# Kernel optimization log

Measured on AMD Instinct MI355X. Metric: run time of the kernel, lower is better.

Reference implementation:

```python
import jax, jax.numpy as jnp
import numpy as np

D_MODEL = 384
N_HEADS = 8
HEAD_DIM = D_MODEL // N_HEADS


def setup_inputs() -> dict:
    key = jax.random.key(0)
    ks = jax.random.split(key, 8)
    b, n = 2, 2048
    s = 0.02
    return {
        "x": jax.random.normal(ks[0], (b, n, D_MODEL), jnp.float32),
        "coords": jax.random.normal(ks[1], (b, n, 3), jnp.float32),
        "W_qkv": jax.random.normal(ks[2], (D_MODEL, 3 * D_MODEL), jnp.float32) * s,
        "b_qkv": jnp.zeros((3 * D_MODEL,), jnp.float32),
        "W_dist": jax.random.normal(ks[3], (1, N_HEADS), jnp.float32) * s,
        "b_dist": jnp.zeros((N_HEADS,), jnp.float32),
        "W_out": jax.random.normal(ks[4], (D_MODEL, D_MODEL), jnp.float32) * s,
        "b_out": jnp.zeros((D_MODEL,), jnp.float32),
    }


def reference(x, coords, W_qkv, b_qkv, W_dist, b_dist, W_out, b_out):
    b, n, _ = x.shape
    qkv = x @ W_qkv + b_qkv                       # (b, n, 3*d)
    q, k, v = jnp.split(qkv, 3, axis=-1)
    def heads(t):
        return t.reshape(b, n, N_HEADS, HEAD_DIM).transpose(0, 2, 1, 3)  # b h n d
    q, k, v = heads(q), heads(k), heads(v)
    attn = jnp.einsum('bhid,bhjd->bhij', q, k) / jnp.sqrt(jnp.float32(HEAD_DIM))
    # distance bias: ||c_i - c_j|| projected to heads (Linear(1, n_heads))
    diff = coords[:, :, None, :] - coords[:, None, :, :]   # (b, i, j, 3)
    dist = jnp.sqrt(jnp.sum(diff * diff, axis=-1))         # (b, i, j)
    dist_bias = dist[..., None] * W_dist[0] + b_dist       # (b, i, j, h)
    attn = attn + dist_bias.transpose(0, 3, 1, 2)          # (b, h, i, j)
    attn = jax.nn.softmax(attn, axis=-1)
    out = jnp.einsum('bhij,bhjd->bhid', attn, v)
    out = out.transpose(0, 2, 1, 3).reshape(b, n, D_MODEL)
    return out @ W_out + b_out
```

## Files before the change

### kernel.cpp

```cpp
#include <hip/hip_runtime.h>
#include <hip/hip_bf16.h>

#define NB 2
#define SEQ 2048
#define DM 384
#define NH 8
#define HD 48
#define QKVN 1152
#define BH (NB*NH)
#define NSPLIT 4

typedef __hip_bfloat16 bf16;
typedef __attribute__((ext_vector_type(8))) short short8;
typedef __attribute__((ext_vector_type(4))) float float4v;

static __device__ __forceinline__ float bf2f(bf16 v){ return __bfloat162float(v); }
static __device__ __forceinline__ float ldin(const void* p, size_t i, int isf){
    return isf ? ((const float*)p)[i] : bf2f(((const bf16*)p)[i]);
}
static __device__ __forceinline__ short f2b(float f){
    union { float f; unsigned u; } a; a.f = f;
    unsigned r = a.u + 0x7FFFu + ((a.u >> 16) & 1u);
    return (short)(r >> 16);
}
static __device__ __forceinline__ unsigned pk2(float a, float b){
    union { float f; unsigned u; } ua, ub; ua.f = a; ub.f = b;
    return ((ua.u + 0x8000u) >> 16) | ((ub.u + 0x8000u) & 0xFFFF0000u);
}
static __device__ __forceinline__ float bflo(unsigned u){
    union { unsigned u; float f; } a; a.u = u << 16; return a.f;
}
static __device__ __forceinline__ float bfhi(unsigned u){
    union { unsigned u; float f; } a; a.u = u & 0xFFFF0000u; return a.f;
}
static __device__ __forceinline__ float bfs(unsigned short s){
    union { unsigned u; float f; } a; a.u = ((unsigned)s) << 16; return a.f;
}
static __device__ __forceinline__ int detect_isf(const void* x){
    const unsigned short* xb = (const unsigned short*)x;
    int l = threadIdx.x & 63;
    union { unsigned u; float f; } a; a.u = ((unsigned)xb[2*l]) << 16;
    float ab = fabsf(a.f);
    int good = (a.f == 0.0f) || (ab > 9.765625e-4f && ab < 1024.0f);
    unsigned long long m = __ballot(good);
    return (__popcll(m) >= 32) ? 0 : 1;
}

__global__ __launch_bounds__(256) void k_prep(const void* __restrict__ x,
    const void* __restrict__ coords,
    const void* __restrict__ Wqkv, const void* __restrict__ Wout,
    const void* __restrict__ bqkv, const void* __restrict__ bout,
    const void* __restrict__ Wdist, const void* __restrict__ bdist,
    short* __restrict__ dist8, short* __restrict__ xb,
    short* __restrict__ WqT, short* __restrict__ WoT,
    float* __restrict__ bqf, float* __restrict__ bof,
    float* __restrict__ wdf, float* __restrict__ bdf)
{
    const int isf = detect_isf(x);
    const int t = threadIdx.x;
    const int b = blockIdx.x;
    if (b < 512) {
        const int bb = b >> 8;
        const int j0 = (b & 255) * 8;
        __shared__ float cjx[8], cjy[8], cjz[8];
        if (t < 8) {
            int gj = (bb*SEQ + j0 + t)*3;
            cjx[t] = ldin(coords, gj, isf);
            cjy[t] = ldin(coords, gj+1, isf);
            cjz[t] = ldin(coords, gj+2, isf);
        }
        __syncthreads();
        #pragma unroll
        for (int ii = 0; ii < 8; ++ii) {
            int i = ii*256 + t;
            int gi = (bb*SEQ + i)*3;
            float px = ldin(coords, gi, isf), py = ldin(coords, gi+1, isf), pz = ldin(coords, gi+2, isf);
            short o[8];
            #pragma unroll
            for (int e = 0; e < 8; ++e) {
                float dx = px - cjx[e], dy = py - cjy[e], dz = pz - cjz[e];
                o[e] = f2b(sqrtf(dx*dx + dy*dy + dz*dz));
            }
            *(int4*)(dist8 + ((size_t)b*SEQ + i)*8) = *(const int4*)o;
        }
    } else if (b < 1280) {
        size_t i = ((size_t)(b-512)*256 + t)*8;
        if (isf) {
            const float* xf = (const float*)x + i;
            short o[8];
            #pragma unroll
            for (int e = 0; e < 8; ++e) o[e] = f2b(xf[e]);
            *(int4*)(xb + i) = *(const int4*)o;
        } else {
            *(int4*)(xb + i) = *(const int4*)((const short*)x + i);
        }
    } else if (b < 1856) {
        int bb, NW; const void* W; short* WT;
        if (b < 1712) { bb = b - 1280; NW = QKVN; W = Wqkv; WT = WqT; }
        else          { bb = b - 1712; NW = DM;   W = Wout; WT = WoT; }
        int ntiles = NW >> 5;
        int kt = bb / ntiles, nt = bb % ntiles;
        int k0 = kt*32, n0 = nt*32;
        __shared__ float Ls[32][33];
        for (int idx = t; idx < 1024; idx += 256) {
            int r = idx >> 5, c = idx & 31;
            Ls[r][c] = ldin(W, (size_t)(k0+r)*NW + n0 + c, isf);
        }
        __syncthreads();
        for (int idx = t; idx < 1024; idx += 256) {
            int r2 = idx >> 5, c2 = idx & 31;
            WT[(size_t)(n0+r2)*DM + k0 + c2] = f2b(Ls[c2][r2]);
        }
    } else {
        int idx = (b - 1856)*256 + t;
        if (idx < QKVN) bqf[idx] = ldin(bqkv, idx, isf);
        else if (idx < QKVN + DM) bof[idx - QKVN] = ldin(bout, idx - QKVN, isf);
        else if (idx < QKVN + DM + NH) wdf[idx - QKVN - DM] = ldin(Wdist, idx - QKVN - DM, isf);
        else if (idx < QKVN + DM + 2*NH) bdf[idx - QKVN - DM - NH] = ldin(bdist, idx - QKVN - DM - NH, isf);
    }
}

__global__ __launch_bounds__(256) void k_qkv(const short* __restrict__ xb,
    const short* __restrict__ WT, const float* __restrict__ bias,
    short* __restrict__ qg2, short* __restrict__ kg2, short* __restrict__ vg2)
{
    __shared__ __align__(16) short As[64*72];
    __shared__ __align__(16) short Bs[128*72];
    const int t = threadIdx.x;
    const int w = t >> 6, lane = t & 63, L = lane & 15, quad = lane >> 4;
    const int mt = blockIdx.x / 9, nt = blockIdx.x % 9;
    const int row0 = mt*64, col0 = nt*128;
    const int wm = w & 1, wn = w >> 1;
    float4v acc[2][4] = {};
    for (int k0 = 0; k0 < DM; k0 += 64) {
        __syncthreads();
        for (int c = t; c < 512; c += 256) {
            int row = c >> 3, k8 = c & 7;
            *(int4*)(&As[row*72 + k8*8]) = *(const int4*)(xb + (size_t)(row0+row)*DM + k0 + k8*8);
        }
        for (int c = t; c < 1024; c += 256) {
            int row = c >> 3, k8 = c & 7;
            *(int4*)(&Bs[row*72 + k8*8]) = *(const int4*)(WT + (size_t)(col0+row)*DM + k0 + k8*8);
        }
        __syncthreads();
        #pragma unroll
        for (int kc = 0; kc < 2; ++kc) {
            short8 a0 = *(const short8*)(&As[(32*wm + L)*72 + kc*32 + quad*8]);
            short8 a1 = *(const short8*)(&As[(32*wm + 16 + L)*72 + kc*32 + quad*8]);
            #pragma unroll
            for (int ni = 0; ni < 4; ++ni) {
                short8 bf = *(const short8*)(&Bs[(64*wn + 16*ni + L)*72 + kc*32 + quad*8]);
                acc[0][ni] = __builtin_amdgcn_mfma_f32_16x16x32_bf16(a0, bf, acc[0][ni], 0, 0, 0);
                acc[1][ni] = __builtin_amdgcn_mfma_f32_16x16x32_bf16(a1, bf, acc[1][ni], 0, 0, 0);
            }
        }
    }
    const int which = col0 / DM;
    const int cbase = col0 % DM;
    short* Ep = Bs;
    __syncthreads();
    if (which < 2) {
        #pragma unroll
        for (int mi = 0; mi < 2; ++mi)
            #pragma unroll
            for (int ni = 0; ni < 4; ++ni) {
                int col_l = 64*wn + 16*ni + L;
                float bv = bias[col0 + col_l];
                #pragma unroll
                for (int r = 0; r < 4; ++r) {
                    int row_l = 32*wm + 16*mi + quad*4 + r;
                    Ep[row_l*136 + col_l] = f2b(acc[mi][ni][r] + bv);
                }
            }
        __syncthreads();
        short* dst = which ? kg2 : qg2;
        for (int c = t; c < 1024; c += 256) {
            int row_l = c >> 4, col_l = (c & 15)*8;
            int4 val = *(const int4*)(&Ep[row_l*136 + col_l]);
            int row_g = row0 + row_l;
            int bi = row_g >> 11, nn = row_g & (SEQ-1);
            int c2 = cbase + col_l;
            int hh = c2/HD, dd = c2%HD;
            int bh = bi*NH + hh;
            size_t u = ((((size_t)bh*128 + (nn>>4))*2 + (dd>>5))*4 + ((dd>>3)&3))*128
                       + (size_t)(nn & 15)*8;
            *(int4*)(dst + u) = val;
        }
    } else {
        #pragma unroll
        for (int mi = 0; mi < 2; ++mi)
            #pragma unroll
            for (int ni = 0; ni < 4; ++ni) {
                int col_l = 64*wn + 16*ni + L;
                float bv = bias[col0 + col_l];
                #pragma unroll
                for (int r = 0; r < 4; ++r) {
                    int row_l = 32*wm + 16*mi + quad*4 + r;
                    Ep[col_l*72 + row_l] = f2b(acc[mi][ni][r] + bv);
                }
            }
        __syncthreads();
        for (int c = t; c < 1024; c += 256) {
            int col_l = c >> 3, row_l = (c & 7)*8;
            int4 val = *(const int4*)(&Ep[col_l*72 + row_l]);
            int row_g = row0 + row_l;
            int bi = row_g >> 11, nn = row_g & (SEQ-1);
            int c2 = cbase + col_l;
            int hh = c2/HD, dd = c2%HD;
            int bh = bi*NH + hh;
            size_t u = (((((size_t)bh*32 + (nn>>6))*3 + (dd>>4))*2 + ((nn>>5)&1))*4 + ((nn>>3)&3))*128
                       + (size_t)(dd & 15)*8;
            *(int4*)(vg2 + u) = val;
        }
    }
}

__global__ __launch_bounds__(256, 4) void k_attn(
    const short* __restrict__ qg2, const short* __restrict__ kg2, const short* __restrict__ vg2,
    const short* __restrict__ dist8, const float* __restrict__ wdf,
    const float* __restrict__ bdf, short* __restrict__ partO, float* __restrict__ partL)
{
    __shared__ __align__(16) short PsT[4][16*72];
    const int t = threadIdx.x;
    const int w = t >> 6, lane = t & 63, L = lane & 15, q = lane >> 4;
    const int bid = blockIdx.x;
    const int jsb = bid & 3, it = (bid >> 2) & 31, bh = bid >> 7;
    const int bi = bh >> 3, hh = bh & 7;
    const int i0 = it*64;
    const float scale = 0.14433756729740643f;
    const float wd = wdf[hh], bd = bdf[hh];

    const short* qbase = qg2 + (((size_t)bh*128 + it*4 + w)*2)*512;
    const short8 qa0 = *(const short8*)(qbase + (q*16 + L)*8);
    const short8 qa1 = *(const short8*)(qbase + 512 + (q*16 + L)*8);

    const int iL = i0 + 16*w + L;
    float rsum = 0.f;
    float4v accO[3] = {};

    const size_t kBH = (size_t)bh*131072;
    const size_t vBH = (size_t)bh*98304;
    const size_t dB  = (size_t)bi*256*SEQ*8;

    const int jlo = jsb*(SEQ/NSPLIT), jhi = jlo + SEQ/NSPLIT;
    for (int j0 = jlo; j0 < jhi; j0 += 64) {
        float4v sacc[4] = {};
        #pragma unroll
        for (int nt = 0; nt < 4; ++nt) {
            const short* kb = kg2 + kBH + ((size_t)((j0>>4) + nt))*1024;
            short8 kf0 = *(const short8*)(kb + (q*16 + L)*8);
            sacc[nt] = __builtin_amdgcn_mfma_f32_16x16x32_bf16(kf0, qa0, sacc[nt], 0, 0, 0);
            short8 kf1 = *(const short8*)(kb + 512 + (q*16 + L)*8);
            sacc[nt] = __builtin_amdgcn_mfma_f32_16x16x32_bf16(kf1, qa1, sacc[nt], 0, 0, 0);
        }
        #pragma unroll
        for (int nt = 0; nt < 4; ++nt) {
            const short* dp = dist8 + dB + (((size_t)(j0>>6)*8 + 2*nt + (q>>1))*SEQ + iL)*8 + 4*(q&1);
            uint2 du = *(const uint2*)dp;
            float d0 = bflo(du.x), d1 = bfhi(du.x), d2 = bflo(du.y), d3 = bfhi(du.y);
            float p0 = __expf(fmaf(sacc[nt][0], scale, fmaf(d0, wd, bd)));
            float p1 = __expf(fmaf(sacc[nt][1], scale, fmaf(d1, wd, bd)));
            float p2 = __expf(fmaf(sacc[nt][2], scale, fmaf(d2, wd, bd)));
            float p3 = __expf(fmaf(sacc[nt][3], scale, fmaf(d3, wd, bd)));
            rsum += (p0 + p1) + (p2 + p3);
            uint2 pw; pw.x = pk2(p0, p1); pw.y = pk2(p2, p3);
            *(uint2*)(&PsT[w][L*72 + 16*nt + 4*q]) = pw;
        }
        short8 pa0 = *(const short8*)(&PsT[w][L*72 + q*8]);
        short8 pa1 = *(const short8*)(&PsT[w][L*72 + 32 + q*8]);
        #pragma unroll
        for (int dt = 0; dt < 3; ++dt) {
            const short* vb = vg2 + vBH + ((size_t)(j0>>6)*3 + dt)*1024;
            short8 vf0 = *(const short8*)(vb + (q*16 + L)*8);
            accO[dt] = __builtin_amdgcn_mfma_f32_16x16x32_bf16(pa0, vf0, accO[dt], 0, 0, 0);
            short8 vf1 = *(const short8*)(vb + 512 + (q*16 + L)*8);
            accO[dt] = __builtin_amdgcn_mfma_f32_16x16x32_bf16(pa1, vf1, accO[dt], 0, 0, 0);
        }
    }
    rsum += __shfl_xor(rsum, 16);
    rsum += __shfl_xor(rsum, 32);
    const size_t pbase = ((size_t)(jsb*BH + bh))*SEQ;
    if (q == 0) partL[pbase + iL] = rsum;
    #pragma unroll
    for (int dt = 0; dt < 3; ++dt)
        #pragma unroll
        for (int r = 0; r < 4; ++r)
            partO[(pbase + i0 + 16*w + 4*q + r)*48 + 16*dt + L] = f2b(accO[dt][r]);
}

__global__ __launch_bounds__(256) void k_red(const short* __restrict__ partO,
    const float* __restrict__ partL, short* __restrict__ aob)
{
    int g = blockIdx.x*256 + threadIdx.x;
    int row = g / 48, cg = g % 48;
    int bi = row >> 11, i = row & (SEQ-1);
    int hh = cg / 6, d8 = (cg % 6)*8;
    int bh = bi*NH + hh;
    float acc[8] = {};
    float l = 0.f;
    #pragma unroll
    for (int s = 0; s < NSPLIT; ++s) {
        const short* p = partO + ((size_t)(s*BH + bh)*SEQ + i)*48 + d8;
        uint4 u = *(const uint4*)p;
        acc[0] += bflo(u.x); acc[1] += bfhi(u.x);
        acc[2] += bflo(u.y); acc[3] += bfhi(u.y);
        acc[4] += bflo(u.z); acc[5] += bfhi(u.z);
        acc[6] += bflo(u.w); acc[7] += bfhi(u.w);
        l += partL[(size_t)(s*BH + bh)*SEQ + i];
    }
    float inv = 1.0f / l;
    short o[8];
    #pragma unroll
    for (int e = 0; e < 8; ++e) o[e] = f2b(acc[e]*inv);
    *(int4*)(aob + (size_t)row*DM + hh*HD + d8) = *(const int4*)o;
}

__global__ __launch_bounds__(256) void k_out(const short* __restrict__ aob,
    const short* __restrict__ WT, const float* __restrict__ bias,
    void* __restrict__ out, const void* __restrict__ x)
{
    __shared__ __align__(16) short As[64*72];
    __shared__ __align__(16) short Bs[128*72];
    const int isf = detect_isf(x);
    const int t = threadIdx.x;
    const int w = t >> 6, lane = t & 63, L = lane & 15, quad = lane >> 4;
    const int mt = blockIdx.x / 3, nt = blockIdx.x % 3;
    const int row0 = mt*64, col0 = nt*128;
    const int wm = w & 1, wn = w >> 1;
    float4v acc[2][4] = {};
    for (int k0 = 0; k0 < DM; k0 += 64) {
        __syncthreads();
        for (int c = t; c < 512; c += 256) {
            int row = c >> 3, k8 = c & 7;
            *(int4*)(&As[row*72 + k8*8]) = *(const int4*)(aob + (size_t)(row0+row)*DM + k0 + k8*8);
        }
        for (int c = t; c < 1024; c += 256) {
            int row = c >> 3, k8 = c & 7;
            *(int4*)(&Bs[row*72 + k8*8]) = *(const int4*)(WT + (size_t)(col0+row)*DM + k0 + k8*8);
        }
        __syncthreads();
        #pragma unroll
        for (int kc = 0; kc < 2; ++kc) {
            short8 a0 = *(const short8*)(&As[(32*wm + L)*72 + kc*32 + quad*8]);
            short8 a1 = *(const short8*)(&As[(32*wm + 16 + L)*72 + kc*32 + quad*8]);
            #pragma unroll
            for (int ni = 0; ni < 4; ++ni) {
                short8 bf = *(const short8*)(&Bs[(64*wn + 16*ni + L)*72 + kc*32 + quad*8]);
                acc[0][ni] = __builtin_amdgcn_mfma_f32_16x16x32_bf16(a0, bf, acc[0][ni], 0, 0, 0);
                acc[1][ni] = __builtin_amdgcn_mfma_f32_16x16x32_bf16(a1, bf, acc[1][ni], 0, 0, 0);
            }
        }
    }
    #pragma unroll
    for (int mi = 0; mi < 2; ++mi) {
        #pragma unroll
        for (int ni = 0; ni < 4; ++ni) {
            int col_g = col0 + 64*wn + 16*ni + L;
            float bv = bias[col_g];
            #pragma unroll
            for (int r = 0; r < 4; ++r) {
                int row_g = row0 + 32*wm + 16*mi + quad*4 + r;
                size_t oi = (size_t)row_g*DM + col_g;
                float val = acc[mi][ni][r] + bv;
                if (isf) ((float*)out)[oi] = val;
                else     ((bf16*)out)[oi]  = __float2bfloat16(val);
            }
        }
    }
}

extern "C" void kernel_launch(void* const* d_in, const int* in_sizes, int n_in,
                              void* d_out, int out_size, void* d_ws, size_t ws_size,
                              hipStream_t stream) {
    const void* x      = d_in[0];
    const void* coords = d_in[1];
    const void* Wqkv   = d_in[2];
    const void* bqkv   = d_in[3];
    const void* Wdist  = d_in[4];
    const void* bdist  = d_in[5];
    const void* Wout   = d_in[6];
    const void* bout   = d_in[7];

    short* qg2   = (short*)d_ws;
    short* kg2   = qg2  + (size_t)2097152;
    short* vg2   = kg2  + (size_t)2097152;
    short* dist8 = vg2  + (size_t)1572864;
    short* aob   = dist8 + (size_t)8388608;
    short* xb    = aob  + (size_t)1572864;
    short* WqT   = xb   + (size_t)1572864;
    short* WoT   = WqT  + (size_t)442368;
    short* partO = WoT  + (size_t)147456;
    float* partL = (float*)(partO + (size_t)NSPLIT*BH*SEQ*48);
    float* bqf   = partL + (size_t)NSPLIT*BH*SEQ;
    float* bof   = bqf + QKVN;
    float* wdf   = bof + DM;
    float* bdf   = wdf + NH;

    hipMemsetAsync(qg2, 0, (size_t)2*2097152*sizeof(short), stream);

    k_prep<<<dim3(1863), dim3(256), 0, stream>>>(x, coords, Wqkv, Wout, bqkv, bout,
                                                 Wdist, bdist, dist8, xb, WqT, WoT,
                                                 bqf, bof, wdf, bdf);
    k_qkv<<<dim3(64*9), dim3(256), 0, stream>>>(xb, WqT, bqf, qg2, kg2, vg2);
    k_attn<<<dim3(16*32*NSPLIT), dim3(256), 0, stream>>>(qg2, kg2, vg2, dist8, wdf, bdf,
                                                         partO, partL);
    k_red<<<dim3(768), dim3(256), 0, stream>>>(partO, partL, aob);
    k_out<<<dim3(64*3), dim3(256), 0, stream>>>(aob, WoT, bof, d_out, x);
}
```

Baseline: 165.8 us.

## Restructure attention: K-stationary waves, packed 48-dim layouts, exp2, LDS cross-wave reduction

Rewrites the attention kernel so each wave owns a distinct slice of keys and loops over all four 16-query tiles, keeping Q fragments in registers. The outputs of the four waves are then summed through shared memory. Q/K/V move to a compact layout where the last 16 of the 48 head dims sit in a zero-padded half-K MFMA operand, which removes the padding memset and the LDS round-trip for P. The dist layout changes to 16 keys per block, and exp is replaced by exp2 with log2e folded into the scale and the distance weights. The cost is more register pressure (occupancy hint lowered to 3), an extra multi-step LDS reduction with barriers, and wasted MFMA work on the zero-padded half.

New measurement: 165.8 us. No clear change (-0.1%).

```diff
diff --git a/kernel.cpp b/kernel.cpp
--- a/kernel.cpp
+++ b/kernel.cpp
@@ -33,8 +33,15 @@
 static __device__ __forceinline__ float bfhi(unsigned u){
     union { unsigned u; float f; } a; a.u = u & 0xFFFF0000u; return a.f;
 }
-static __device__ __forceinline__ float bfs(unsigned short s){
-    union { unsigned u; float f; } a; a.u = ((unsigned)s) << 16; return a.f;
+static __device__ __forceinline__ short8 s4z(int2 v){
+    union { int2 i; short s[4]; } u; u.i = v;
+    short8 r = {u.s[0], u.s[1], u.s[2], u.s[3], 0, 0, 0, 0};
+    return r;
+}
+static __device__ __forceinline__ short8 u2z(unsigned a, unsigned b){
+    union { unsigned u[2]; short s[4]; } u0; u0.u[0] = a; u0.u[1] = b;
+    short8 r = {u0.s[0], u0.s[1], u0.s[2], u0.s[3], 0, 0, 0, 0};
+    return r;
 }
 static __device__ __forceinline__ int detect_isf(const void* x){
     const unsigned short* xb = (const unsigned short*)x;
@@ -59,11 +66,11 @@
     const int isf = detect_isf(x);
     const int t = threadIdx.x;
     const int b = blockIdx.x;
-    if (b < 512) {
-        const int bb = b >> 8;
-        const int j0 = (b & 255) * 8;
-        __shared__ float cjx[8], cjy[8], cjz[8];
-        if (t < 8) {
+    if (b < 256) {
+        const int bb = b >> 7;
+        const int j0 = (b & 127) * 16;
+        __shared__ float cjx[16], cjy[16], cjz[16];
+        if (t < 16) {
             int gj = (bb*SEQ + j0 + t)*3;
             cjx[t] = ldin(coords, gj, isf);
             cjy[t] = ldin(coords, gj+1, isf);
@@ -71,20 +78,22 @@
         }
         __syncthreads();
         #pragma unroll
-        for (int ii = 0; ii < 8; ++ii) {
-            int i = ii*256 + t;
+        for (int k = 0; k < 8; ++k) {
+            int i = k*256 + t;
             int gi = (bb*SEQ + i)*3;
             float px = ldin(coords, gi, isf), py = ldin(coords, gi+1, isf), pz = ldin(coords, gi+2, isf);
-            short o[8];
-            #pragma unroll
-            for (int e = 0; e < 8; ++e) {
+            short o[16];
+            #pragma unroll
+            for (int e = 0; e < 16; ++e) {
                 float dx = px - cjx[e], dy = py - cjy[e], dz = pz - cjz[e];
                 o[e] = f2b(sqrtf(dx*dx + dy*dy + dz*dz));
             }
-            *(int4*)(dist8 + ((size_t)b*SEQ + i)*8) = *(const int4*)o;
-        }
-    } else if (b < 1280) {
-        size_t i = ((size_t)(b-512)*256 + t)*8;
+            short* dst = dist8 + ((size_t)b*SEQ + i)*16;
+            *(int4*)dst       = *(const int4*)(o);
+            *(int4*)(dst + 8) = *(const int4*)(o + 8);
+        }
+    } else if (b < 1024) {
+        size_t i = ((size_t)(b-256)*256 + t)*8;
         if (isf) {
             const float* xf = (const float*)x + i;
             short o[8];
@@ -94,10 +103,10 @@
         } else {
             *(int4*)(xb + i) = *(const int4*)((const short*)x + i);
         }
-    } else if (b < 1856) {
+    } else if (b < 1600) {
         int bb, NW; const void* W; short* WT;
-        if (b < 1712) { bb = b - 1280; NW = QKVN; W = Wqkv; WT = WqT; }
-        else          { bb = b - 1712; NW = DM;   W = Wout; WT = WoT; }
+        if (b < 1456) { bb = b - 1024; NW = QKVN; W = Wqkv; WT = WqT; }
+        else          { bb = b - 1456; NW = DM;   W = Wout; WT = WoT; }
         int ntiles = NW >> 5;
         int kt = bb / ntiles, nt = bb % ntiles;
         int k0 = kt*32, n0 = nt*32;
@@ -112,11 +121,12 @@
             WT[(size_t)(n0+r2)*DM + k0 + c2] = f2b(Ls[c2][r2]);
         }
     } else {
-        int idx = (b - 1856)*256 + t;
+        int idx = (b - 1600)*256 + t;
+        const float log2e = 1.4426950408889634f;
         if (idx < QKVN) bqf[idx] = ldin(bqkv, idx, isf);
         else if (idx < QKVN + DM) bof[idx - QKVN] = ldin(bout, idx - QKVN, isf);
-        else if (idx < QKVN + DM + NH) wdf[idx - QKVN - DM] = ldin(Wdist, idx - QKVN - DM, isf);
-        else if (idx < QKVN + DM + 2*NH) bdf[idx - QKVN - DM - NH] = ldin(bdist, idx - QKVN - DM - NH, isf);
+        else if (idx < QKVN + DM + NH) wdf[idx - QKVN - DM] = ldin(Wdist, idx - QKVN - DM, isf)*log2e;
+        else if (idx < QKVN + DM + 2*NH) bdf[idx - QKVN - DM - NH] = ldin(bdist, idx - QKVN - DM - NH, isf)*log2e;
     }
 }
 
@@ -176,15 +186,21 @@
         short* dst = which ? kg2 : qg2;
         for (int c = t; c < 1024; c += 256) {
             int row_l = c >> 4, col_l = (c & 15)*8;
-            int4 val = *(const int4*)(&Ep[row_l*136 + col_l]);
             int row_g = row0 + row_l;
             int bi = row_g >> 11, nn = row_g & (SEQ-1);
             int c2 = cbase + col_l;
-            int hh = c2/HD, dd = c2%HD;
+            int hh = c2/HD, dh = c2%HD;
             int bh = bi*NH + hh;
-            size_t u = ((((size_t)bh*128 + (nn>>4))*2 + (dd>>5))*4 + ((dd>>3)&3))*128
-                       + (size_t)(nn & 15)*8;
-            *(int4*)(dst + u) = val;
+            size_t base = ((size_t)bh*128 + (nn>>4))*768;
+            int Ltok = nn & 15;
+            const short* src = &Ep[row_l*136 + col_l];
+            if (dh < 32) {
+                *(int4*)(dst + base + (dh>>3)*128 + Ltok*8) = *(const int4*)src;
+            } else {
+                int q0 = (dh - 32) >> 2;
+                *(int2*)(dst + base + 512 + q0*64     + Ltok*4) = *(const int2*)src;
+                *(int2*)(dst + base + 512 + (q0+1)*64 + Ltok*4) = *(const int2*)(src + 4);
+            }
         }
     } else {
         #pragma unroll
@@ -201,91 +217,150 @@
             }
         __syncthreads();
         for (int c = t; c < 1024; c += 256) {
-            int col_l = c >> 3, row_l = (c & 7)*8;
-            int4 val = *(const int4*)(&Ep[col_l*72 + row_l]);
-            int row_g = row0 + row_l;
+            int col_l = c >> 3, row8 = (c & 7)*8;
+            int row_g = row0 + row8;
             int bi = row_g >> 11, nn = row_g & (SEQ-1);
             int c2 = cbase + col_l;
-            int hh = c2/HD, dd = c2%HD;
+            int hh = c2/HD, dh = c2%HD;
             int bh = bi*NH + hh;
-            size_t u = (((((size_t)bh*32 + (nn>>6))*3 + (dd>>4))*2 + ((nn>>5)&1))*4 + ((nn>>3)&3))*128
-                       + (size_t)(dd & 15)*8;
-            *(int4*)(vg2 + u) = val;
-        }
-    }
-}
-
-__global__ __launch_bounds__(256, 4) void k_attn(
+            int dt = dh >> 4, Lh = dh & 15;
+            size_t base3 = (((size_t)bh*128 + (nn>>4))*3 + dt)*256;
+            int q0 = (nn & 15) >> 2;
+            const short* src = &Ep[col_l*72 + row8];
+            *(int2*)(vg2 + base3 + q0*64     + Lh*4) = *(const int2*)src;
+            *(int2*)(vg2 + base3 + (q0+1)*64 + Lh*4) = *(const int2*)(src + 4);
+        }
+    }
+}
+
+__global__ __launch_bounds__(256, 3) void k_attn(
     const short* __restrict__ qg2, const short* __restrict__ kg2, const short* __restrict__ vg2,
     const short* __restrict__ dist8, const float* __restrict__ wdf,
     const float* __restrict__ bdf, short* __restrict__ partO, float* __restrict__ partL)
 {
-    __shared__ __align__(16) short PsT[4][16*72];
+    __shared__ float Ored[2][64*48];
+    __shared__ float Lred[2][64];
     const int t = threadIdx.x;
     const int w = t >> 6, lane = t & 63, L = lane & 15, q = lane >> 4;
     const int bid = blockIdx.x;
     const int jsb = bid & 3, it = (bid >> 2) & 31, bh = bid >> 7;
     const int bi = bh >> 3, hh = bh & 7;
     const int i0 = it*64;
-    const float scale = 0.14433756729740643f;
+    const float scale2 = 0.14433756729740643f * 1.4426950408889634f;
     const float wd = wdf[hh], bd = bdf[hh];
 
-    const short* qbase = qg2 + (((size_t)bh*128 + it*4 + w)*2)*512;
-    const short8 qa0 = *(const short8*)(qbase + (q*16 + L)*8);
-    const short8 qa1 = *(const short8*)(qbase + 512 + (q*16 + L)*8);
-
-    const int iL = i0 + 16*w + L;
-    float rsum = 0.f;
-    float4v accO[3] = {};
-
-    const size_t kBH = (size_t)bh*131072;
-    const size_t vBH = (size_t)bh*98304;
-    const size_t dB  = (size_t)bi*256*SEQ*8;
-
-    const int jlo = jsb*(SEQ/NSPLIT), jhi = jlo + SEQ/NSPLIT;
-    for (int j0 = jlo; j0 < jhi; j0 += 64) {
+    const short* qB = qg2 + ((size_t)bh*128 + it*4)*768;
+    short8 qa0[4], qa1[4];
+    #pragma unroll
+    for (int nt = 0; nt < 4; ++nt) {
+        qa0[nt] = *(const short8*)(qB + nt*768 + q*128 + L*8);
+        qa1[nt] = s4z(*(const int2*)(qB + nt*768 + 512 + q*64 + L*4));
+    }
+
+    float4v accO[4][3] = {};
+    float rsum[4] = {};
+
+    const short* kBp = kg2 + ((size_t)bh*128 + jsb*32 + w)*768;
+    const short* vBp = vg2 + ((size_t)bh*128 + jsb*32 + w)*768;
+    const short* dBp = dist8 + (((size_t)bi*128 + jsb*32 + w)*SEQ + i0 + L)*16 + 4*q;
+
+    #pragma unroll 2
+    for (int itr = 0; itr < SEQ/NSPLIT/64; ++itr) {
+        short8 ka0 = *(const short8*)(kBp + q*128 + L*8);
+        short8 ka1 = s4z(*(const int2*)(kBp + 512 + q*64 + L*4));
         float4v sacc[4] = {};
         #pragma unroll
         for (int nt = 0; nt < 4; ++nt) {
-            const short* kb = kg2 + kBH + ((size_t)((j0>>4) + nt))*1024;
-            short8 kf0 = *(const short8*)(kb + (q*16 + L)*8);
-            sacc[nt] = __builtin_amdgcn_mfma_f32_16x16x32_bf16(kf0, qa0, sacc[nt], 0, 0, 0);
-            short8 kf1 = *(const short8*)(kb + 512 + (q*16 + L)*8);
-            sacc[nt] = __builtin_amdgcn_mfma_f32_16x16x32_bf16(kf1, qa1, sacc[nt], 0, 0, 0);
-        }
+            sacc[nt] = __builtin_amdgcn_mfma_f32_16x16x32_bf16(ka0, qa0[nt], sacc[nt], 0, 0, 0);
+            sacc[nt] = __builtin_amdgcn_mfma_f32_16x16x32_bf16(ka1, qa1[nt], sacc[nt], 0, 0, 0);
+        }
+        short8 vf[3];
+        #pragma unroll
+        for (int dt = 0; dt < 3; ++dt)
+            vf[dt] = s4z(*(const int2*)(vBp + dt*256 + q*64 + L*4));
+        short8 pa[4];
         #pragma unroll
         for (int nt = 0; nt < 4; ++nt) {
-            const short* dp = dist8 + dB + (((size_t)(j0>>6)*8 + 2*nt + (q>>1))*SEQ + iL)*8 + 4*(q&1);
-            uint2 du = *(const uint2*)dp;
-            float d0 = bflo(du.x), d1 = bfhi(du.x), d2 = bflo(du.y), d3 = bfhi(du.y);
-            float p0 = __expf(fmaf(sacc[nt][0], scale, fmaf(d0, wd, bd)));
-            float p1 = __expf(fmaf(sacc[nt][1], scale, fmaf(d1, wd, bd)));
-            float p2 = __expf(fmaf(sacc[nt][2], scale, fmaf(d2, wd, bd)));
-            float p3 = __expf(fmaf(sacc[nt][3], scale, fmaf(d3, wd, bd)));
-            rsum += (p0 + p1) + (p2 + p3);
-            uint2 pw; pw.x = pk2(p0, p1); pw.y = pk2(p2, p3);
-            *(uint2*)(&PsT[w][L*72 + 16*nt + 4*q]) = pw;
-        }
-        short8 pa0 = *(const short8*)(&PsT[w][L*72 + q*8]);
-        short8 pa1 = *(const short8*)(&PsT[w][L*72 + 32 + q*8]);
-        #pragma unroll
-        for (int dt = 0; dt < 3; ++dt) {
-            const short* vb = vg2 + vBH + ((size_t)(j0>>6)*3 + dt)*1024;
-            short8 vf0 = *(const short8*)(vb + (q*16 + L)*8);
-            accO[dt] = __builtin_amdgcn_mfma_f32_16x16x32_bf16(pa0, vf0, accO[dt], 0, 0, 0);
-            short8 vf1 = *(const short8*)(vb + 512 + (q*16 + L)*8);
-            accO[dt] = __builtin_amdgcn_mfma_f32_16x16x32_bf16(pa1, vf1, accO[dt], 0, 0, 0);
-        }
-    }
-    rsum += __shfl_xor(rsum, 16);
-    rsum += __shfl_xor(rsum, 32);
-    const size_t pbase = ((size_t)(jsb*BH + bh))*SEQ;
-    if (q == 0) partL[pbase + iL] = rsum;
+            int2 du = *(const int2*)(dBp + nt*256);
+            float d0 = bflo((unsigned)du.x), d1 = bfhi((unsigned)du.x);
+            float d2 = bflo((unsigned)du.y), d3 = bfhi((unsigned)du.y);
+            float p0 = __builtin_amdgcn_exp2f(fmaf(sacc[nt][0], scale2, fmaf(d0, wd, bd)));
+            float p1 = __builtin_amdgcn_exp2f(fmaf(sacc[nt][1], scale2, fmaf(d1, wd, bd)));
+            float p2 = __builtin_amdgcn_exp2f(fmaf(sacc[nt][2], scale2, fmaf(d2, wd, bd)));
+            float p3 = __builtin_amdgcn_exp2f(fmaf(sacc[nt][3], scale2, fmaf(d3, wd, bd)));
+            rsum[nt] += (p0 + p1) + (p2 + p3);
+            pa[nt] = u2z(pk2(p0, p1), pk2(p2, p3));
+        }
+        #pragma unroll
+        for (int nt = 0; nt < 4; ++nt)
+            #pragma unroll
+            for (int dt = 0; dt < 3; ++dt)
+                accO[nt][dt] = __builtin_amdgcn_mfma_f32_16x16x32_bf16(pa[nt], vf[dt], accO[nt][dt], 0, 0, 0);
+        kBp += 4*768; vBp += 4*768; dBp += (size_t)4*SEQ*16;
+    }
     #pragma unroll
-    for (int dt = 0; dt < 3; ++dt)
-        #pragma unroll
-        for (int r = 0; r < 4; ++r)
-            partO[(pbase + i0 + 16*w + 4*q + r)*48 + 16*dt + L] = f2b(accO[dt][r]);
+    for (int nt = 0; nt < 4; ++nt) {
+        rsum[nt] += __shfl_xor(rsum[nt], 16);
+        rsum[nt] += __shfl_xor(rsum[nt], 32);
+    }
+    if (w >= 2) {
+        float* Od = Ored[w-2];
+        #pragma unroll
+        for (int mt = 0; mt < 4; ++mt)
+            #pragma unroll
+            for (int dt = 0; dt < 3; ++dt)
+                #pragma unroll
+                for (int r = 0; r < 4; ++r)
+                    Od[(16*mt + 4*q + r)*48 + 16*dt + L] = accO[mt][dt][r];
+        if (q == 0)
+            #pragma unroll
+            for (int nt = 0; nt < 4; ++nt) Lred[w-2][16*nt + L] = rsum[nt];
+    }
+    __syncthreads();
+    if (w < 2) {
+        float* Od = Ored[w];
+        #pragma unroll
+        for (int mt = 0; mt < 4; ++mt)
+            #pragma unroll
+            for (int dt = 0; dt < 3; ++dt)
+                #pragma unroll
+                for (int r = 0; r < 4; ++r)
+                    accO[mt][dt][r] += Od[(16*mt + 4*q + r)*48 + 16*dt + L];
+        #pragma unroll
+        for (int nt = 0; nt < 4; ++nt) rsum[nt] += Lred[w][16*nt + L];
+    }
+    __syncthreads();
+    if (w == 1) {
+        float* Od = Ored[0];
+        #pragma unroll
+        for (int mt = 0; mt < 4; ++mt)
+            #pragma unroll
+            for (int dt = 0; dt < 3; ++dt)
+                #pragma unroll
+                for (int r = 0; r < 4; ++r)
+                    Od[(16*mt + 4*q + r)*48 + 16*dt + L] = accO[mt][dt][r];
+        if (q == 0)
+            #pragma unroll
+            for (int nt = 0; nt < 4; ++nt) Lred[0][16*nt + L] = rsum[nt];
+    }
+    __syncthreads();
+    if (w == 0) {
+        float* Od = Ored[0];
+        const size_t pbase = ((size_t)(jsb*BH + bh))*SEQ;
+        #pragma unroll
+        for (int mt = 0; mt < 4; ++mt)
+            #pragma unroll
+            for (int dt = 0; dt < 3; ++dt)
+                #pragma unroll
+                for (int r = 0; r < 4; ++r) {
+                    float v = accO[mt][dt][r] + Od[(16*mt + 4*q + r)*48 + 16*dt + L];
+                    partO[(pbase + i0 + 16*mt + 4*q + r)*48 + 16*dt + L] = f2b(v);
+                }
+        if (q == 0)
+            #pragma unroll
+            for (int nt = 0; nt < 4; ++nt)
+                partL[pbase + i0 + 16*nt + L] = rsum[nt] + Lred[0][16*nt + L];
+    }
 }
 
 __global__ __launch_bounds__(256) void k_red(const short* __restrict__ partO,
@@ -382,23 +457,21 @@
     const void* bout   = d_in[7];
 
     short* qg2   = (short*)d_ws;
-    short* kg2   = qg2  + (size_t)2097152;
-    short* vg2   = kg2  + (size_t)2097152;
+    short* kg2   = qg2  + (size_t)1572864;
+    short* vg2   = kg2  + (size_t)1572864;
     short* dist8 = vg2  + (size_t)1572864;
     short* aob   = dist8 + (size_t)8388608;
     short* xb    = aob  + (size_t)1572864;
     short* WqT   = xb   + (size_t)1572864;
     short* WoT   = WqT  + (size_t)442368;
     short* partO = WoT  + (size_t)147456;
-    float* partL = (float*)(partO + (size_t)NSPLIT*BH*SEQ*48);
-    float* bqf   = partL + (size_t)NSPLIT*BH*SEQ;
+    float* partL = (float*)(partO + (size_t)6291456);
+    float* bqf   = partL + (size_t)131072;
     float* bof   = bqf + QKVN;
     float* wdf   = bof + DM;
     float* bdf   = wdf + NH;
 
-    hipMemsetAsync(qg2, 0, (size_t)2*2097152*sizeof(short), stream);
-
-    k_prep<<<dim3(1863), dim3(256), 0, stream>>>(x, coords, Wqkv, Wout, bqkv, bout,
+    k_prep<<<dim3(1607), dim3(256), 0, stream>>>(x, coords, Wqkv, Wout, bqkv, bout,
                                                  Wdist, bdist, dist8, xb, WqT, WoT,
                                                  bqf, bof, wdf, bdf);
     k_qkv<<<dim3(64*9), dim3(256), 0, stream>>>(xb, WqT, bqf, qg2, kg2, vg2);
```
